# Optimization experiments

Hardware: AMD Instinct MI355X
Metric: run time of the kernel (lower is better)

Reference implementation:

```python
import jax, jax.numpy as jnp
import numpy as np

R = 14        # num_relations
N = 100000    # num nodes
E = 1600000   # num edges
B = 8         # n_bases: num_blocks for layer 1, num_bases for layer 2
DIN, DH, DOUT = 64, 64, 64


def setup_inputs() -> dict:
    key = jax.random.key(0)
    ks = jax.random.split(key, 10)
    x = jax.random.normal(ks[0], (N, DIN), jnp.float32)
    edge_index = jax.random.randint(ks[1], (2, E), 0, N)
    edge_type = jax.random.randint(ks[2], (E,), 0, R)
    # Layer 1: block-diagonal decomposition weights (R, B, DIN/B, DH/B)
    w1 = jax.random.normal(ks[3], (R, B, DIN // B, DH // B), jnp.float32) * 0.1
    root1 = jax.random.normal(ks[4], (DIN, DH), jnp.float32) * 0.1
    bias1 = jnp.zeros((DH,), jnp.float32)
    # Layer 2: basis decomposition: W_r = sum_b comp2[r,b] * bases2[b]
    comp2 = jax.random.normal(ks[5], (R, B), jnp.float32) * 0.3
    bases2 = jax.random.normal(ks[6], (B, DH, DOUT), jnp.float32) * 0.1
    root2 = jax.random.normal(ks[7], (DH, DOUT), jnp.float32) * 0.1
    bias2 = jnp.zeros((DOUT,), jnp.float32)
    return {"x": x, "edge_index": edge_index, "edge_type": edge_type,
            "w1": w1, "root1": root1, "bias1": bias1,
            "comp2": comp2, "bases2": bases2, "root2": root2, "bias2": bias2}


def _rel_scatter_max(h_rel, src, dst, edge_type):
    """h_rel: (R, N, d) per-relation transformed node features.
    Per-relation scatter-max over destination nodes, then sum over relations
    (PyG RGCNConv with aggr='max': empty segments contribute 0)."""
    msgs = h_rel[edge_type, src]                  # (E, d) gather
    seg = edge_type * N + dst                     # combined (relation, dst) key
    agg = jax.ops.segment_max(msgs, seg, num_segments=R * N)  # (R*N, d), -inf where empty
    agg = jnp.where(jnp.isneginf(agg), 0.0, agg)
    return agg.reshape(R, N, -1).sum(axis=0)      # (N, d)


def reference(x, edge_index, edge_type, w1, root1, bias1, comp2, bases2, root2, bias2):
    src, dst = edge_index[0], edge_index[1]
    # ---- layer 1: block-diagonal RGCNConv, aggr='max' ----
    xb = x.reshape(N, B, DIN // B)
    h = jnp.einsum('nbi,rbio->rnbo', xb, w1).reshape(R, N, DH)
    out = _rel_scatter_max(h, src, dst, edge_type) + x @ root1 + bias1
    x1 = jax.nn.relu(out)  # dropout p=0.4 is identity in eval mode
    # ---- layer 2: basis-decomposed RGCNConv, aggr='max' ----
    W2 = jnp.einsum('rb,bio->rio', comp2, bases2)  # (R, DH, DOUT)
    h2 = jnp.einsum('ni,rio->rno', x1, W2)         # (R, N, DOUT)
    out2 = _rel_scatter_max(h2, src, dst, edge_type) + x1 @ root2 + bias2
    return out2
```

## Files before the change

### kernel.cpp

```cpp
#include <hip/hip_runtime.h>
#include <math.h>

#define RNUM 14
#define NNODE 100000
#define ENUM 1600000
#define NBKT 196
#define NFINE 8192
#define SLOT 9216
#define NBLK1 ((ENUM + 8191) / 8192)
#define NT16 (NNODE / 16)
#define NTB ((NT16 + 15) / 16)
#define FRAGREL (RNUM + 1)
#define FRAGTOT (2 * FRAGREL * 4096)

typedef __attribute__((ext_vector_type(8))) short bf16x8;
typedef __attribute__((ext_vector_type(4))) float f32x4;

__device__ inline unsigned short f2bf(float f) {
    unsigned u = __builtin_bit_cast(unsigned, f);
    u += 0x7FFF + ((u >> 16) & 1);
    return (unsigned short)(u >> 16);
}
__device__ inline float bf2f(unsigned short h) {
    unsigned u = ((unsigned)h) << 16;
    return __builtin_bit_cast(float, u);
}
__device__ inline int uload(const int* __restrict__ p) {
    return __builtin_amdgcn_readfirstlane(*p);
}

__global__ void __launch_bounds__(1024) scatter1_k(const int* __restrict__ src,
        const int* __restrict__ dst, const int* __restrict__ et,
        int* __restrict__ bcur, int2* __restrict__ pay) {
    __shared__ int cnt[256];
    __shared__ int rnk[256];
    __shared__ int base[256];
    int t = threadIdx.x;
    if (t < 256) { cnt[t] = 0; rnk[t] = 0; }
    __syncthreads();
    int e0 = blockIdx.x * 8192;
    int d[8], s[8], r[8];
#pragma unroll
    for (int j = 0; j < 8; j++) {
        int e = e0 + j * 1024 + t;
        if (e < ENUM) {
            d[j] = dst[e]; s[j] = src[e]; r[j] = et[e];
            atomicAdd(&cnt[d[j] >> 9], 1);
        } else d[j] = -1;
    }
    __syncthreads();
    if (t < NBKT && cnt[t] > 0) base[t] = atomicAdd(&bcur[t], cnt[t]);
    __syncthreads();
#pragma unroll
    for (int j = 0; j < 8; j++) {
        if (d[j] < 0) continue;
        int b = d[j] >> 9;
        int rk = atomicAdd(&rnk[b], 1);
        int pos = base[b] + rk;
        if (pos >= SLOT) pos = SLOT - 1;
        int2 p; p.x = r[j] * NNODE + s[j]; p.y = (d[j] & 511) * 16 + r[j];
        pay[(size_t)b * SLOT + pos] = p;
    }
}

__global__ void __launch_bounds__(1024) bsort_k(const int2* __restrict__ pay,
        const int* __restrict__ bcur, int* __restrict__ offs, int* __restrict__ ssrc) {
    __shared__ int cnt[NFINE];
    __shared__ int tsum[1024];
    int bkt = blockIdx.x, t = threadIdx.x;
    int e0 = bkt * SLOT;
    int ecnt = uload(bcur + bkt);
#pragma unroll
    for (int i = t; i < NFINE; i += 1024) cnt[i] = 0;
    __syncthreads();
    for (int e = t; e < ecnt; e += 1024) atomicAdd(&cnt[pay[(size_t)e0 + e].y], 1);
    __syncthreads();
    int loc[8], s = 0;
#pragma unroll
    for (int j = 0; j < 8; j++) { loc[j] = cnt[t * 8 + j]; s += loc[j]; }
    tsum[t] = s;
    __syncthreads();
    for (int o = 1; o < 1024; o <<= 1) {
        int u = (t >= o) ? tsum[t - o] : 0;
        __syncthreads();
        tsum[t] += u;
        __syncthreads();
    }
    int run = tsum[t] - s;
#pragma unroll
    for (int j = 0; j < 8; j++) {
        int idx = t * 8 + j;
        cnt[idx] = run;
        offs[bkt * NFINE + idx] = e0 + run;
        run += loc[j];
    }
    __syncthreads();
    for (int e = t; e < ecnt; e += 1024) {
        int2 p = pay[(size_t)e0 + e];
        int rk = atomicAdd(&cnt[p.y], 1);
        ssrc[e0 + rk] = p.x;
    }
}

__global__ void prep_k(const float* __restrict__ w1, const float* __restrict__ comp2,
                       const float* __restrict__ bases2, const float* __restrict__ root1,
                       const float* __restrict__ root2, const float* __restrict__ x,
                       unsigned short* __restrict__ frag1, unsigned short* __restrict__ frag2,
                       unsigned short* __restrict__ xb) {
    int gid = blockIdx.x * 256 + threadIdx.x;
    if (gid < FRAGTOT) {
        int half = gid >= FRAGREL * 4096;
        int idx = gid - half * (FRAGREL * 4096);
        int j = idx & 7, lane = (idx >> 3) & 63, ot = (idx >> 9) & 3, kh = (idx >> 11) & 1, r = idx >> 12;
        int k = kh * 32 + (lane >> 4) * 8 + j;
        int c = ot * 16 + (lane & 15);
        float v;
        if (!half) {
            if (r < RNUM) {
                int bi = k >> 3, bo = c >> 3;
                v = 0.f;
                if (bi == bo) v = w1[((r * 8 + bi) * 8 + (k & 7)) * 8 + (c & 7)];
            } else v = root1[k * 64 + c];
            frag1[idx] = f2bf(v);
        } else {
            if (r < RNUM) {
                float s = 0.f;
#pragma unroll
                for (int b = 0; b < 8; b++) s += comp2[r * 8 + b] * bases2[(b * 64 + k) * 64 + c];
                v = s;
            } else v = root2[k * 64 + c];
            frag2[idx] = f2bf(v);
        }
    } else {
        int idx = gid - FRAGTOT;
        if (idx < NNODE * 64) xb[idx] = f2bf(x[idx]);
    }
}

template <int TSTORE>
__global__ void __launch_bounds__(256) gemm_k(const unsigned short* __restrict__ A,
                                              const unsigned short* __restrict__ F,
                                              const unsigned short* __restrict__ Froot,
                                              unsigned short* __restrict__ H,
                                              unsigned short* __restrict__ xrootb,
                                              int nrel) {
    __shared__ unsigned short tl[4][16][72];
    int tb = blockIdx.x % NTB;
    int r  = blockIdx.x / NTB;
    bool isroot = (r == nrel);
    const unsigned short* Fr = isroot ? Froot : F + (size_t)r * 4096;
    int wave = threadIdx.x >> 6, lane = threadIdx.x & 63;
    bf16x8 wf[2][4];
#pragma unroll
    for (int kh = 0; kh < 2; kh++)
#pragma unroll
        for (int ot = 0; ot < 4; ot++)
            wf[kh][ot] = *(const bf16x8*)(Fr + ((kh * 4 + ot) * 64 + lane) * 8);
    int node16 = lane & 15;
    int kcol = (lane >> 4) * 8;
    int g = lane >> 4;
    unsigned short* Ybase = isroot ? xrootb : H + (size_t)r * NNODE * 64;
    for (int s = 0; s < 4; s++) {
        int nt = tb * 16 + wave * 4 + s;
        if (nt >= NT16) break;
        int nbase = nt * 16;
        const unsigned short* Arow = A + (size_t)(nbase + node16) * 64;
        bf16x8 b0 = *(const bf16x8*)(Arow + kcol);
        bf16x8 b1 = *(const bf16x8*)(Arow + 32 + kcol);
        f32x4 acc[4];
#pragma unroll
        for (int ot = 0; ot < 4; ot++) {
            acc[ot] = (f32x4){0.f, 0.f, 0.f, 0.f};
            acc[ot] = __builtin_amdgcn_mfma_f32_16x16x32_bf16(wf[0][ot], b0, acc[ot], 0, 0, 0);
            acc[ot] = __builtin_amdgcn_mfma_f32_16x16x32_bf16(wf[1][ot], b1, acc[ot], 0, 0, 0);
        }
        unsigned short* Yr = Ybase + (size_t)nbase * 64;
        if constexpr (TSTORE) {
#pragma unroll
            for (int ot = 0; ot < 4; ot++) {
                uint2 pv;
                pv.x = (unsigned)f2bf(acc[ot][0]) | ((unsigned)f2bf(acc[ot][1]) << 16);
                pv.y = (unsigned)f2bf(acc[ot][2]) | ((unsigned)f2bf(acc[ot][3]) << 16);
                *(uint2*)&tl[wave][node16][ot * 16 + g * 4] = pv;
            }
#pragma unroll
            for (int q = 0; q < 2; q++) {
                int nd = q * 8 + (lane >> 3);
                int ch = (lane & 7) * 8;
                uint4 v = *(uint4*)&tl[wave][nd][ch];
                *(uint4*)(Yr + (size_t)nd * 64 + ch) = v;
            }
        } else {
#pragma unroll
            for (int ot = 0; ot < 4; ot++) {
                uint2 pv;
                pv.x = (unsigned)f2bf(acc[ot][0]) | ((unsigned)f2bf(acc[ot][1]) << 16);
                pv.y = (unsigned)f2bf(acc[ot][2]) | ((unsigned)f2bf(acc[ot][3]) << 16);
                *(uint2*)(Yr + (size_t)node16 * 64 + ot * 16 + g * 4) = pv;
            }
        }
    }
}

template <bool NT>
__device__ inline float hload(const unsigned short* __restrict__ p) {
    unsigned short v = NT ? __builtin_nontemporal_load(p) : *p;
    return bf2f(v);
}

template <int RC, bool NT>
__global__ void __launch_bounds__(256) agg_k(
    const unsigned short* __restrict__ H, const int* __restrict__ offs,
    const int* __restrict__ ssrc, const unsigned short* __restrict__ xrootb,
    const float* __restrict__ bias, float* __restrict__ aggbuf,
    unsigned short* __restrict__ x1b, float* __restrict__ outf,
    int r0, int r0N, int rcnt, int flags) {
    int wv = threadIdx.x >> 6, lane = threadIdx.x & 63;
    int d = __builtin_amdgcn_readfirstlane(blockIdx.x * 4 + wv);
    if (d >= NNODE) return;
    float msum = 0.f;

    if constexpr (RC > 0) {
        const int base = d * 16 + r0;
        int bnd[RC + 1];
#pragma unroll
        for (int j = 0; j <= RC; j++) bnd[j] = offs[base + j];
        int e0   = __builtin_amdgcn_readfirstlane(bnd[0]);
        int eend = __builtin_amdgcn_readfirstlane(bnd[RC]);
        float m = -INFINITY;
        for (int cb = e0; cb < eend; cb += 64) {
            int idx = cb + lane;
            int cidx = (idx < eend) ? idx : eend - 1;
            int sv = ssrc[cidx];
            unsigned long long mask = 0;
#pragma unroll
            for (int j = 1; j < RC; j++) {
                int kk_ = bnd[j] - cb;
                if (kk_ >= 0 && kk_ < 64 && bnd[j] > e0) mask |= 1ull << kk_;
            }
            int n = eend - cb; if (n > 64) n = 64;
            for (int k0 = 0; k0 < n; k0 += 16) {
                float h[16];
#pragma unroll
                for (int u = 0; u < 16; u++) {
                    int kk = k0 + u;
                    int kc = (kk < n) ? kk : n - 1;
                    int s = __builtin_amdgcn_readlane(sv, kc);
                    h[u] = hload<NT>(H + (size_t)(s - r0N) * 64 + lane);
                }
#pragma unroll
                for (int u = 0; u < 16; u++) {
                    int kk = k0 + u;
                    if (kk >= n) break;
                    bool fl = (mask >> kk) & 1;
                    msum += fl ? m : 0.f;
                    m = fl ? h[u] : fmaxf(m, h[u]);
                }
            }
        }
        if (eend > e0) msum += m;
    } else {
        const int base = d * 16 + r0;
        for (int j = 0; j < rcnt; j++) {
            int e = uload(offs + base + j);
            int ee = uload(offs + base + j + 1);
            if (e >= ee) continue;
            float m = -INFINITY;
            for (; e < ee; e++) {
                int s = uload(ssrc + e);
                m = fmaxf(m, bf2f(H[(size_t)(s - r0N) * 64 + lane]));
            }
            msum += m;
        }
    }

    size_t o = (size_t)d * 64 + lane;
    if (!(flags & 1)) msum += aggbuf[o];
    if (!(flags & 2)) { aggbuf[o] = msum; return; }
    float v = msum + bf2f(xrootb[o]) + bias[lane];
    if (flags & 4) x1b[o] = f2bf(fmaxf(v, 0.f));
    else outf[o] = v;
}

extern "C" void kernel_launch(void* const* d_in, const int* in_sizes, int n_in,
                              void* d_out, int out_size, void* d_ws, size_t ws_size,
                              hipStream_t stream) {
    const float* x      = (const float*)d_in[0];
    const int*   ei     = (const int*)d_in[1];
    const int*   et     = (const int*)d_in[2];
    const float* w1     = (const float*)d_in[3];
    const float* root1  = (const float*)d_in[4];
    const float* bias1  = (const float*)d_in[5];
    const float* comp2  = (const float*)d_in[6];
    const float* bases2 = (const float*)d_in[7];
    const float* root2  = (const float*)d_in[8];
    const float* bias2  = (const float*)d_in[9];
    const int* srcv = ei;
    const int* dstv = ei + ENUM;
    float* out = (float*)d_out;

    char* w = (char*)d_ws;
    size_t off = 0;
    auto alloc = [&](size_t bytes) -> void* {
        void* p = w + off;
        off += (bytes + 255) & ~(size_t)255;
        return p;
    };
    int*   offs = (int*)alloc(((size_t)NBKT * NFINE + 1) * sizeof(int));
    int*   bcur = (int*)alloc(256 * sizeof(int));
    int2*  pay  = (int2*)alloc((size_t)NBKT * SLOT * sizeof(int2));
    int*   ssrc = (int*)alloc((size_t)NBKT * SLOT * sizeof(int));
    unsigned short* xb     = (unsigned short*)alloc((size_t)NNODE * 64 * 2);
    unsigned short* xrootb = (unsigned short*)alloc((size_t)NNODE * 64 * 2);
    unsigned short* frag1  = (unsigned short*)alloc((size_t)FRAGREL * 4096 * 2);
    unsigned short* frag2  = (unsigned short*)alloc((size_t)FRAGREL * 4096 * 2);
    size_t fixed = off;
    if (fixed > ws_size) return;
    size_t slab = ((size_t)NNODE * 64 * 2 + 255) & ~(size_t)255;
    size_t avail = ws_size - fixed;
    int r_per;
    float* aggbuf;
    unsigned short* H;
    if (avail >= (size_t)RNUM * slab) {
        r_per = RNUM;
        H = (unsigned short*)alloc((size_t)RNUM * slab);
        aggbuf = (float*)H;
    } else {
        aggbuf = (float*)alloc((size_t)NNODE * 64 * 4);
        if (off > ws_size) return;
        avail = ws_size - off;
        r_per = (int)(avail / slab);
        if (r_per < 1) return;
        if (r_per > RNUM) r_per = RNUM;
        H = (unsigned short*)alloc((size_t)r_per * slab);
    }

    hipMemsetAsync(bcur, 0, 256 * sizeof(int), stream);

    scatter1_k<<<NBLK1, 1024, 0, stream>>>(srcv, dstv, et, bcur, pay);
    bsort_k<<<NBKT, 1024, 0, stream>>>(pay, bcur, offs, ssrc);

    prep_k<<<(FRAGTOT + NNODE * 64 + 255) / 256, 256, 0, stream>>>(
        w1, comp2, bases2, root1, root2, x, frag1, frag2, xb);

    int nch = (RNUM + r_per - 1) / r_per;
    int aggGrid = NNODE / 4;

    for (int layer = 0; layer < 2; layer++) {
        const unsigned short* frag = layer ? frag2 : frag1;
        const unsigned short* rootf = (layer ? frag2 : frag1) + (size_t)RNUM * 4096;
        const float* bias = layer ? bias2 : bias1;
        for (int c = 0; c < nch; c++) {
            int r0 = c * r_per;
            int rcnt = (RNUM - r0 < r_per) ? (RNUM - r0) : r_per;
            int grid = (c == 0) ? (rcnt + 1) * NTB : rcnt * NTB;
            if (layer == 0)
                gemm_k<1><<<grid, 256, 0, stream>>>(xb, frag + (size_t)r0 * 4096, rootf,
                                                    H, xrootb, rcnt);
            else
                gemm_k<0><<<grid, 256, 0, stream>>>(xb, frag + (size_t)r0 * 4096, rootf,
                                                    H, xrootb, rcnt);
            int flags = (c == 0 ? 1 : 0) | (c == nch - 1 ? 2 : 0) | (layer == 0 ? 4 : 0);
            if (rcnt == RNUM) {
                if (layer == 0)
                    agg_k<RNUM, true><<<aggGrid, 256, 0, stream>>>(H, offs, ssrc, xrootb, bias,
                                                                   aggbuf, xb, out, r0, r0 * NNODE, rcnt, flags);
                else
                    agg_k<RNUM, false><<<aggGrid, 256, 0, stream>>>(H, offs, ssrc, xrootb, bias,
                                                                    aggbuf, xb, out, r0, r0 * NNODE, rcnt, flags);
            } else {
                agg_k<0, false><<<aggGrid, 256, 0, stream>>>(H, offs, ssrc, xrootb, bias,
                                                             aggbuf, xb, out, r0, r0 * NNODE, rcnt, flags);
            }
        }
    }
}
```

Baseline: 388.0 us.

## Fuse prep into scatter kernel, vectorize offs loads, unify gemm/agg templates

Folds the weight-fragment and bf16 conversion prep work into extra blocks of the edge scatter kernel, so one launch is removed and the prep overlaps with the edge bucketing. The gemm always uses the LDS-transposed coalesced store, and the nontemporal load variant in aggregation is dropped. Aggregation now loads segment boundaries with int4 vector loads. It also clamps the bucket count to SLOT and derives NBKT from the key range. These edits trade a few specialisations for fewer kernel variants and launches.

```diff
diff --git a/kernel.cpp b/kernel.cpp
--- a/kernel.cpp
+++ b/kernel.cpp
@@ -4,10 +4,12 @@
 #define RNUM 14
 #define NNODE 100000
 #define ENUM 1600000
-#define NBKT 196
+#define NKEY (NNODE * 16)
+#define NBKT ((NKEY + 8191) / 8192)
 #define NFINE 8192
 #define SLOT 9216
 #define NBLK1 ((ENUM + 8191) / 8192)
+#define PREPB 128
 #define NT16 (NNODE / 16)
 #define NTB ((NT16 + 15) / 16)
 #define FRAGREL (RNUM + 1)
@@ -31,11 +33,49 @@
 
 __global__ void __launch_bounds__(1024) scatter1_k(const int* __restrict__ src,
         const int* __restrict__ dst, const int* __restrict__ et,
-        int* __restrict__ bcur, int2* __restrict__ pay) {
+        int* __restrict__ bcur, int2* __restrict__ pay,
+        const float* __restrict__ w1, const float* __restrict__ comp2,
+        const float* __restrict__ bases2, const float* __restrict__ root1,
+        const float* __restrict__ root2, const float* __restrict__ x,
+        unsigned short* __restrict__ frag1, unsigned short* __restrict__ frag2,
+        unsigned short* __restrict__ xb) {
+    int t = threadIdx.x;
+    if ((int)blockIdx.x >= NBLK1) {
+        const int TOT = FRAGTOT + NNODE * 64;
+        for (int gid = ((int)blockIdx.x - NBLK1) * 1024 + t; gid < TOT; gid += PREPB * 1024) {
+            if (gid < FRAGTOT) {
+                int half = gid >= FRAGREL * 4096;
+                int idx = gid - half * (FRAGREL * 4096);
+                int j = idx & 7, lane = (idx >> 3) & 63, ot = (idx >> 9) & 3, kh = (idx >> 11) & 1, r = idx >> 12;
+                int k = kh * 32 + (lane >> 4) * 8 + j;
+                int c = ot * 16 + (lane & 15);
+                float v;
+                if (!half) {
+                    if (r < RNUM) {
+                        int bi = k >> 3, bo = c >> 3;
+                        v = 0.f;
+                        if (bi == bo) v = w1[((r * 8 + bi) * 8 + (k & 7)) * 8 + (c & 7)];
+                    } else v = root1[k * 64 + c];
+                    frag1[idx] = f2bf(v);
+                } else {
+                    if (r < RNUM) {
+                        float s = 0.f;
+#pragma unroll
+                        for (int b = 0; b < 8; b++) s += comp2[r * 8 + b] * bases2[(b * 64 + k) * 64 + c];
+                        v = s;
+                    } else v = root2[k * 64 + c];
+                    frag2[idx] = f2bf(v);
+                }
+            } else {
+                int idx = gid - FRAGTOT;
+                xb[idx] = f2bf(x[idx]);
+            }
+        }
+        return;
+    }
     __shared__ int cnt[256];
     __shared__ int rnk[256];
     __shared__ int base[256];
-    int t = threadIdx.x;
     if (t < 256) { cnt[t] = 0; rnk[t] = 0; }
     __syncthreads();
     int e0 = blockIdx.x * 8192;
@@ -70,6 +110,7 @@
     int bkt = blockIdx.x, t = threadIdx.x;
     int e0 = bkt * SLOT;
     int ecnt = uload(bcur + bkt);
+    if (ecnt > SLOT) ecnt = SLOT;
 #pragma unroll
     for (int i = t; i < NFINE; i += 1024) cnt[i] = 0;
     __syncthreads();
@@ -102,42 +143,6 @@
     }
 }
 
-__global__ void prep_k(const float* __restrict__ w1, const float* __restrict__ comp2,
-                       const float* __restrict__ bases2, const float* __restrict__ root1,
-                       const float* __restrict__ root2, const float* __restrict__ x,
-                       unsigned short* __restrict__ frag1, unsigned short* __restrict__ frag2,
-                       unsigned short* __restrict__ xb) {
-    int gid = blockIdx.x * 256 + threadIdx.x;
-    if (gid < FRAGTOT) {
-        int half = gid >= FRAGREL * 4096;
-        int idx = gid - half * (FRAGREL * 4096);
-        int j = idx & 7, lane = (idx >> 3) & 63, ot = (idx >> 9) & 3, kh = (idx >> 11) & 1, r = idx >> 12;
-        int k = kh * 32 + (lane >> 4) * 8 + j;
-        int c = ot * 16 + (lane & 15);
-        float v;
-        if (!half) {
-            if (r < RNUM) {
-                int bi = k >> 3, bo = c >> 3;
-                v = 0.f;
-                if (bi == bo) v = w1[((r * 8 + bi) * 8 + (k & 7)) * 8 + (c & 7)];
-            } else v = root1[k * 64 + c];
-            frag1[idx] = f2bf(v);
-        } else {
-            if (r < RNUM) {
-                float s = 0.f;
-#pragma unroll
-                for (int b = 0; b < 8; b++) s += comp2[r * 8 + b] * bases2[(b * 64 + k) * 64 + c];
-                v = s;
-            } else v = root2[k * 64 + c];
-            frag2[idx] = f2bf(v);
-        }
-    } else {
-        int idx = gid - FRAGTOT;
-        if (idx < NNODE * 64) xb[idx] = f2bf(x[idx]);
-    }
-}
-
-template <int TSTORE>
 __global__ void __launch_bounds__(256) gemm_k(const unsigned short* __restrict__ A,
                                               const unsigned short* __restrict__ F,
                                               const unsigned short* __restrict__ Froot,
@@ -174,41 +179,25 @@
             acc[ot] = __builtin_amdgcn_mfma_f32_16x16x32_bf16(wf[0][ot], b0, acc[ot], 0, 0, 0);
             acc[ot] = __builtin_amdgcn_mfma_f32_16x16x32_bf16(wf[1][ot], b1, acc[ot], 0, 0, 0);
         }
+#pragma unroll
+        for (int ot = 0; ot < 4; ot++) {
+            uint2 pv;
+            pv.x = (unsigned)f2bf(acc[ot][0]) | ((unsigned)f2bf(acc[ot][1]) << 16);
+            pv.y = (unsigned)f2bf(acc[ot][2]) | ((unsigned)f2bf(acc[ot][3]) << 16);
+            *(uint2*)&tl[wave][node16][ot * 16 + g * 4] = pv;
+        }
         unsigned short* Yr = Ybase + (size_t)nbase * 64;
-        if constexpr (TSTORE) {
-#pragma unroll
-            for (int ot = 0; ot < 4; ot++) {
-                uint2 pv;
-                pv.x = (unsigned)f2bf(acc[ot][0]) | ((unsigned)f2bf(acc[ot][1]) << 16);
-                pv.y = (unsigned)f2bf(acc[ot][2]) | ((unsigned)f2bf(acc[ot][3]) << 16);
-                *(uint2*)&tl[wave][node16][ot * 16 + g * 4] = pv;
-            }
-#pragma unroll
-            for (int q = 0; q < 2; q++) {
-                int nd = q * 8 + (lane >> 3);
-                int ch = (lane & 7) * 8;
-                uint4 v = *(uint4*)&tl[wave][nd][ch];
-                *(uint4*)(Yr + (size_t)nd * 64 + ch) = v;
-            }
-        } else {
-#pragma unroll
-            for (int ot = 0; ot < 4; ot++) {
-                uint2 pv;
-                pv.x = (unsigned)f2bf(acc[ot][0]) | ((unsigned)f2bf(acc[ot][1]) << 16);
-                pv.y = (unsigned)f2bf(acc[ot][2]) | ((unsigned)f2bf(acc[ot][3]) << 16);
-                *(uint2*)(Yr + (size_t)node16 * 64 + ot * 16 + g * 4) = pv;
-            }
-        }
-    }
-}
-
-template <bool NT>
-__device__ inline float hload(const unsigned short* __restrict__ p) {
-    unsigned short v = NT ? __builtin_nontemporal_load(p) : *p;
-    return bf2f(v);
-}
-
-template <int RC, bool NT>
+#pragma unroll
+        for (int q = 0; q < 2; q++) {
+            int nd = q * 8 + (lane >> 3);
+            int ch = (lane & 7) * 8;
+            uint4 v = *(uint4*)&tl[wave][nd][ch];
+            *(uint4*)(Yr + (size_t)nd * 64 + ch) = v;
+        }
+    }
+}
+
+template <int RC>
 __global__ void __launch_bounds__(256) agg_k(
     const unsigned short* __restrict__ H, const int* __restrict__ offs,
     const int* __restrict__ ssrc, const unsigned short* __restrict__ xrootb,
@@ -220,13 +209,16 @@
     if (d >= NNODE) return;
     float msum = 0.f;
 
-    if constexpr (RC > 0) {
-        const int base = d * 16 + r0;
-        int bnd[RC + 1];
-#pragma unroll
-        for (int j = 0; j <= RC; j++) bnd[j] = offs[base + j];
+    if constexpr (RC == RNUM) {
+        const int base = d * 16;
+        int4 q0 = *(const int4*)(offs + base);
+        int4 q1 = *(const int4*)(offs + base + 4);
+        int4 q2 = *(const int4*)(offs + base + 8);
+        int4 q3 = *(const int4*)(offs + base + 12);
+        int bnd[15] = {q0.x, q0.y, q0.z, q0.w, q1.x, q1.y, q1.z, q1.w,
+                       q2.x, q2.y, q2.z, q2.w, q3.x, q3.y, q3.z};
         int e0   = __builtin_amdgcn_readfirstlane(bnd[0]);
-        int eend = __builtin_amdgcn_readfirstlane(bnd[RC]);
+        int eend = __builtin_amdgcn_readfirstlane(bnd[14]);
         float m = -INFINITY;
         for (int cb = e0; cb < eend; cb += 64) {
             int idx = cb + lane;
@@ -234,7 +226,7 @@
             int sv = ssrc[cidx];
             unsigned long long mask = 0;
 #pragma unroll
-            for (int j = 1; j < RC; j++) {
+            for (int j = 1; j < 14; j++) {
                 int kk_ = bnd[j] - cb;
                 if (kk_ >= 0 && kk_ < 64 && bnd[j] > e0) mask |= 1ull << kk_;
             }
@@ -246,7 +238,7 @@
                     int kk = k0 + u;
                     int kc = (kk < n) ? kk : n - 1;
                     int s = __builtin_amdgcn_readlane(sv, kc);
-                    h[u] = hload<NT>(H + (size_t)(s - r0N) * 64 + lane);
+                    h[u] = bf2f(H[(size_t)s * 64 + lane]);
                 }
 #pragma unroll
                 for (int u = 0; u < 16; u++) {
@@ -337,11 +329,9 @@
 
     hipMemsetAsync(bcur, 0, 256 * sizeof(int), stream);
 
-    scatter1_k<<<NBLK1, 1024, 0, stream>>>(srcv, dstv, et, bcur, pay);
+    scatter1_k<<<NBLK1 + PREPB, 1024, 0, stream>>>(srcv, dstv, et, bcur, pay,
+        w1, comp2, bases2, root1, root2, x, frag1, frag2, xb);
     bsort_k<<<NBKT, 1024, 0, stream>>>(pay, bcur, offs, ssrc);
-
-    prep_k<<<(FRAGTOT + NNODE * 64 + 255) / 256, 256, 0, stream>>>(
-        w1, comp2, bases2, root1, root2, x, frag1, frag2, xb);
 
     int nch = (RNUM + r_per - 1) / r_per;
     int aggGrid = NNODE / 4;
@@ -354,24 +344,15 @@
             int r0 = c * r_per;
             int rcnt = (RNUM - r0 < r_per) ? (RNUM - r0) : r_per;
             int grid = (c == 0) ? (rcnt + 1) * NTB : rcnt * NTB;
-            if (layer == 0)
-                gemm_k<1><<<grid, 256, 0, stream>>>(xb, frag + (size_t)r0 * 4096, rootf,
-                                                    H, xrootb, rcnt);
+            gemm_k<<<grid, 256, 0, stream>>>(xb, frag + (size_t)r0 * 4096, rootf,
+                                             H, xrootb, rcnt);
+            int flags = (c == 0 ? 1 : 0) | (c == nch - 1 ? 2 : 0) | (layer == 0 ? 4 : 0);
+            if (rcnt == RNUM)
+                agg_k<RNUM><<<aggGrid, 256, 0, stream>>>(H, offs, ssrc, xrootb, bias,
+                                                         aggbuf, xb, out, 0, 0, rcnt, flags);
             else
-                gemm_k<0><<<grid, 256, 0, stream>>>(xb, frag + (size_t)r0 * 4096, rootf,
-                                                    H, xrootb, rcnt);
-            int flags = (c == 0 ? 1 : 0) | (c == nch - 1 ? 2 : 0) | (layer == 0 ? 4 : 0);
-            if (rcnt == RNUM) {
-                if (layer == 0)
-                    agg_k<RNUM, true><<<aggGrid, 256, 0, stream>>>(H, offs, ssrc, xrootb, bias,
-                                                                   aggbuf, xb, out, r0, r0 * NNODE, rcnt, flags);
-                else
-                    agg_k<RNUM, false><<<aggGrid, 256, 0, stream>>>(H, offs, ssrc, xrootb, bias,
-                                                                    aggbuf, xb, out, r0, r0 * NNODE, rcnt, flags);
-            } else {
-                agg_k<0, false><<<aggGrid, 256, 0, stream>>>(H, offs, ssrc, xrootb, bias,
-                                                             aggbuf, xb, out, r0, r0 * NNODE, rcnt, flags);
-            }
-        }
-    }
-}
+                agg_k<0><<<aggGrid, 256, 0, stream>>>(H, offs, ssrc, xrootb, bias,
+                                                      aggbuf, xb, out, r0, r0 * NNODE, rcnt, flags);
+        }
+    }
+}
```

After: 376.2 us. -3.0%, faster.
